# Kernel tuning notes

Measured on AMD Instinct MI355X. Metric: run time of the kernel, lower is better.

## Reference

```python
import jax, jax.numpy as jnp
import numpy as np

# Fixed architecture constants (match init_kwargs)
B, CIN, H, W = 2, 3, 224, 224
COUT = 64
KH = KW = 7
SH = SW = 2
PAD = 3
GROUPS = 1
MIX = 4
CG = COUT // GROUPS          # channels per group
REL = CG // 2                # rel_size
PH, PW = H + 2 * PAD, W + 2 * PAD          # padded spatial dims (230, 230)
FH = (PH - KH) // SH + 1                    # output height (112)
FW = (PW - KW) // SW + 1                    # output width  (112)


def setup_inputs() -> dict:
    key = jax.random.key(0)
    ks = jax.random.split(key, 10)
    n = jax.random.normal
    return {
        "x": n(ks[0], (B, CIN, H, W), jnp.float32),
        "weight_query": n(ks[1], (GROUPS, CIN // GROUPS, CG), jnp.float32) * 0.2,
        "weight_key": n(ks[2], (GROUPS, CIN // GROUPS, CG), jnp.float32) * 0.2,
        "weight_value": n(ks[3], (MIX, GROUPS, CIN // GROUPS, CG), jnp.float32) * 0.2,
        "relative_x": n(ks[4], (REL, 1, KW), jnp.float32) * 0.1,
        "relative_y": n(ks[5], (CG - REL, KH, 1), jnp.float32) * 0.1,
        "emb_x": n(ks[6], (CG, 1, PW), jnp.float32) * 0.1,
        "emb_y": n(ks[7], (CG, PH, 1), jnp.float32) * 0.1,
        "emb_m": n(ks[8], (MIX, CG, 1, 1), jnp.float32) * 0.1,
        "bias": n(ks[9], (COUT,), jnp.float32) * 0.05,
    }


def _unfold(t):
    """torch.nn.functional.unfold: (b,c,PH,PW) -> (b,c,KH*KW,FH*FW) with (c,kh,kw) layout."""
    b, c = t.shape[0], t.shape[1]
    ri = jnp.arange(FH) * SH
    rj = jnp.arange(FW) * SW
    p = t[:, :, ri[:, None] + jnp.arange(KH)[None, :], :]          # (b,c,FH,KH,PW)
    p = p[:, :, :, :, rj[:, None] + jnp.arange(KW)[None, :]]       # (b,c,FH,KH,FW,KW)
    return p.transpose(0, 1, 3, 5, 2, 4).reshape(b, c, KH * KW, FH * FW)


def _forward(x, wq, wk, wv, rx, ry, ex, ey, em, bias):
    b = x.shape[0]
    # relative position bias: (COUT, KH*KW, 1)
    rel = jnp.concatenate([jnp.tile(rx, (1, KH, 1)), jnp.tile(ry, (1, 1, KW))], axis=0)
    rel = jnp.tile(rel, (GROUPS, 1, 1)).reshape(COUT, KH * KW, 1)

    xp = jnp.pad(x, ((0, 0), (0, 0), (PAD, PAD), (PAD, PAD)))       # (b,CIN,PH,PW)
    x_ij = xp.transpose(0, 2, 3, 1).reshape(b, PH * PW, GROUPS, CIN // GROUPS)

    # per-pixel grouped projections -> (b, COUT, PH, PW)
    vq = jnp.einsum('bngi,gio->bgon', x_ij, wq).reshape(b, COUT, PH, PW)
    vk = jnp.einsum('bngi,gio->bgon', x_ij, wk).reshape(b, COUT, PH, PW)

    # mixture weights over value transforms: softmax over mix axis, per pixel
    p_ab = ex + ey                                                   # (CG,PH,PW)
    p_abm = jax.nn.softmax(jnp.sum(p_ab[None] * em, axis=1), axis=0) # (MIX,PH,PW)

    vvm = jnp.einsum('bngi,mgio->mbgon', x_ij, wv).reshape(MIX, b, COUT, PH, PW)
    vv = jnp.sum(vvm * p_abm[:, None, None], axis=0)                 # (b,COUT,PH,PW)

    win_k = _unfold(vk)                                              # (b,COUT,KH*KW,L)
    win_v = _unfold(vv)                                              # (b,COUT,KH*KW,L)
    # center query of each window (equivalent to unfold then slice center)
    ci = (KH - 1) // 2 + jnp.arange(FH) * SH
    cj = (KW - 1) // 2 + jnp.arange(FW) * SW
    win_q = vq[:, :, ci[:, None], cj[None, :]].reshape(b, COUT, 1, FH * FW)

    scores = jnp.sum(win_q * (win_k + rel[None]), axis=1)            # (b,KH*KW,L)
    # NOTE: the torch code applies softmax over dim=2 which, after the sum over
    # channels, is the SPATIAL dim (L), not the window dim. Faithful to source.
    attn = jax.nn.softmax(scores, axis=2)                            # (b,KH*KW,L)
    v = jnp.sum(attn[:, None] * win_v, axis=2) + bias[None, :, None] # (b,COUT,L)
    return v.reshape(b, COUT, FH, FW)


def reference(x, weight_query, weight_key, weight_value, relative_x, relative_y, emb_x, emb_y, emb_m, bias):
    return _forward(x, weight_query, weight_key, weight_value, relative_x, relative_y, emb_x, emb_y, emb_m, bias)
```

## Files before the change

### kernel.cpp

```cpp
#include <hip/hip_runtime.h>
#include <math.h>

namespace {
constexpr int Bc = 2, Hc = 224, Wc = 224, HWc = Hc * Wc;
constexpr int COUTc = 64, PADc = 3;
constexpr int MIXc = 4, RELc = 32;
constexpr int PHc = 230, PWc = 230;
constexpr int FHc = 112, FWc = 112, NN = FHc * FWc;
constexpr int NK = 49;
constexpr int CH = 32;
constexpr int NCH = NN / CH;
constexpr int WS_EEX = 0;
constexpr int WS_EEY = WS_EEX + MIXc * PWc;
constexpr int WS_PART = WS_EEY + MIXc * PHc;
constexpr int WS_E = WS_PART + Bc * NK * NCH;
}

__device__ __forceinline__ void collapse(const float* __restrict__ wq,
                                         const float* __restrict__ wk,
                                         const float* __restrict__ rx,
                                         const float* __restrict__ ry,
                                         float* sCol) {
  const int t = threadIdx.x;
  if (t < 51) {
    float s = 0.f;
    if (t < 9) {
      const int cj = t / 3, ci = t % 3;
#pragma unroll 8
      for (int o = 0; o < COUTc; ++o) s += wq[cj * COUTc + o] * wk[ci * COUTc + o];
    } else if (t < 30) {
      const int v = t - 9, cj = v / 7, kw = v % 7;
#pragma unroll 8
      for (int o = 0; o < RELc; ++o) s += wq[cj * COUTc + o] * rx[o * 7 + kw];
    } else {
      const int v = t - 30, cj = v / 7, kh = v % 7;
#pragma unroll 8
      for (int o = 0; o < RELc; ++o) s += wq[cj * COUTc + RELc + o] * ry[o * 7 + kh];
    }
    sCol[t] = s;
  }
}

__global__ __launch_bounds__(256) void sam_scores(
    const float* __restrict__ x, const float* __restrict__ wq,
    const float* __restrict__ wk, const float* __restrict__ rx,
    const float* __restrict__ ry, const float* __restrict__ ex,
    const float* __restrict__ ey, const float* __restrict__ em,
    float* __restrict__ ws) {
  __shared__ float sCol[51];
  const int t = threadIdx.x;
  const int c = blockIdx.x, b = blockIdx.y;
  collapse(wq, wk, rx, ry, sCol);

  const int bf = b * NCH + c;
  if (bf < 8) {
    const int idx = bf * 256 + t;
    constexpr int half = MIXc * PWc;
    if (idx < 2 * half) {
      const int which = idx >= half;
      const int r = which ? idx - half : idx;
      const int m = r / PWc, j = r % PWc;
      float s = 0.f;
#pragma unroll 8
      for (int cc = 0; cc < COUTc; ++cc)
        s += (which ? ey[cc * PHc + j] : ex[cc * PWc + j]) * em[m * COUTc + cc];
      ws[idx] = __expf(s);
    }
  }
  __syncthreads();

  const int g = t >> 5, px = t & 31;
  const int n = c * CH + px;
  const int fh = n / FWc, fw = n - fh * FWc;
  const int i0 = 2 * fh, j0 = 2 * fw;
  const float* xb = x + (size_t)b * 3 * HWc;
  const int co = i0 * Wc + j0;
  const float xc0 = xb[co], xc1 = xb[HWc + co], xc2 = xb[2 * HWc + co];
  const float q0 = xc0 * sCol[0] + xc1 * sCol[3] + xc2 * sCol[6];
  const float q1 = xc0 * sCol[1] + xc1 * sCol[4] + xc2 * sCol[7];
  const float q2 = xc0 * sCol[2] + xc1 * sCol[5] + xc2 * sCol[8];

  float* E = ws + WS_E;
  float* part = ws + WS_PART;
#pragma unroll
  for (int it = 0; it < 7; ++it) {
    const int kk = g + 8 * it;
    if (kk < NK) {
      const int kh = kk / 7, kw = kk - 7 * kh;
      float s = xc0 * (sCol[9 + kw] + sCol[30 + kh]) +
                xc1 * (sCol[16 + kw] + sCol[37 + kh]) +
                xc2 * (sCol[23 + kw] + sCol[44 + kh]);
      const int ir = i0 + kh - PADc, jc = j0 + kw - PADc;
      if ((unsigned)ir < (unsigned)Hc && (unsigned)jc < (unsigned)Wc) {
        const int off = ir * Wc + jc;
        s += q0 * xb[off] + q1 * xb[HWc + off] + q2 * xb[2 * HWc + off];
      }
      const float e = __expf(s);
      E[(size_t)(b * NK + kk) * NN + n] = e;
      float r = e;
      r += __shfl_xor(r, 1, 64);
      r += __shfl_xor(r, 2, 64);
      r += __shfl_xor(r, 4, 64);
      r += __shfl_xor(r, 8, 64);
      r += __shfl_xor(r, 16, 64);
      if (px == 0) part[(b * NK + kk) * NCH + c] = r;
    }
  }
}

__global__ __launch_bounds__(256) void sam_out(
    const float* __restrict__ x, const float* __restrict__ wv,
    const float* __restrict__ bias, const float* __restrict__ ws,
    float* __restrict__ out) {
  __shared__ float sEEX[MIXc * PWc];
  __shared__ float sEEY[MIXc * PHc];
  __shared__ float sdninv[NK];
  __shared__ float swv[12 * 64];
  __shared__ float sbias[64];
  __shared__ float sT[8][32][13];

  const int t = threadIdx.x;
  const int c = blockIdx.x, b = blockIdx.y;
  for (int i = t; i < MIXc * PWc; i += 256) sEEX[i] = ws[WS_EEX + i];
  for (int i = t; i < MIXc * PHc; i += 256) sEEY[i] = ws[WS_EEY + i];
  if (t < 64) sbias[t] = bias[t];
  for (int i = t; i < 12 * 64; i += 256) swv[i] = wv[i];
  if (t < 4 * NK) {
    const int k = t >> 2, p = t & 3;
    const float* base = ws + WS_PART + (b * NK + k) * NCH;
    float s = 0.f;
    for (int cc = p; cc < NCH; cc += 4) s += base[cc];
    s += __shfl_xor(s, 1, 64);
    s += __shfl_xor(s, 2, 64);
    if (p == 0) sdninv[k] = 1.f / s;
  }
  __syncthreads();

  const int g = t >> 5, px = t & 31;
  const int n = c * CH + px;
  const int fh = n / FWc, fw = n - fh * FWc;
  const int i0 = 2 * fh, j0 = 2 * fw;
  const float* xb = x + (size_t)b * 3 * HWc;
  const float* E = ws + WS_E;

  float T[12] = {0.f};
#pragma unroll
  for (int it = 0; it < 7; ++it) {
    const int kk = g + 8 * it;
    if (kk < NK) {
      const int kh = kk / 7, kw = kk - 7 * kh;
      const int ir = i0 + kh - PADc, jc = j0 + kw - PADc;
      if ((unsigned)ir < (unsigned)Hc && (unsigned)jc < (unsigned)Wc) {
        const float e = E[(size_t)(b * NK + kk) * NN + n] * sdninv[kk];
        const int ii = i0 + kh, jj = j0 + kw;
        const float p0 = sEEX[jj] * sEEY[ii];
        const float p1 = sEEX[PWc + jj] * sEEY[PHc + ii];
        const float p2 = sEEX[2 * PWc + jj] * sEEY[2 * PHc + ii];
        const float p3 = sEEX[3 * PWc + jj] * sEEY[3 * PHc + ii];
        const float wgt = e * __builtin_amdgcn_rcpf(p0 + p1 + p2 + p3);
        const int off = ir * Wc + jc;
        const float x0 = xb[off], x1 = xb[HWc + off], x2 = xb[2 * HWc + off];
        const float a0 = wgt * p0, a1 = wgt * p1, a2 = wgt * p2, a3 = wgt * p3;
        T[0] += a0 * x0; T[1]  += a0 * x1; T[2]  += a0 * x2;
        T[3] += a1 * x0; T[4]  += a1 * x1; T[5]  += a1 * x2;
        T[6] += a2 * x0; T[7]  += a2 * x1; T[8]  += a2 * x2;
        T[9] += a3 * x0; T[10] += a3 * x1; T[11] += a3 * x2;
      }
    }
  }
#pragma unroll
  for (int j = 0; j < 12; ++j) sT[g][px][j] = T[j];
  __syncthreads();

  float Tm[12];
#pragma unroll
  for (int j = 0; j < 12; ++j) {
    float s = 0.f;
#pragma unroll
    for (int ww = 0; ww < 8; ++ww) s += sT[ww][px][j];
    Tm[j] = s;
  }
  float* ob = out + (size_t)b * COUTc * NN + n;
#pragma unroll
  for (int oo = 0; oo < 8; ++oo) {
    const int o = g * 8 + oo;
    float acc = sbias[o];
#pragma unroll
    for (int mc = 0; mc < 12; ++mc) acc += swv[mc * 64 + o] * Tm[mc];
    ob[(size_t)o * NN] = acc;
  }
}

extern "C" void kernel_launch(void* const* d_in, const int* in_sizes, int n_in,
                              void* d_out, int out_size, void* d_ws, size_t ws_size,
                              hipStream_t stream) {
  const float* x    = (const float*)d_in[0];
  const float* wq   = (const float*)d_in[1];
  const float* wk   = (const float*)d_in[2];
  const float* wv   = (const float*)d_in[3];
  const float* rx   = (const float*)d_in[4];
  const float* ry   = (const float*)d_in[5];
  const float* ex   = (const float*)d_in[6];
  const float* ey   = (const float*)d_in[7];
  const float* em   = (const float*)d_in[8];
  const float* bias = (const float*)d_in[9];
  float* out = (float*)d_out;
  float* ws  = (float*)d_ws;

  sam_scores<<<dim3(NCH, Bc), 256, 0, stream>>>(x, wq, wk, rx, ry, ex, ey, em, ws);
  sam_out<<<dim3(NCH, Bc), 256, 0, stream>>>(x, wv, bias, ws, out);
}
```

Before: 113.2 us.

## Recompute attention exponentials in output kernel instead of storing them

The stats kernel now only computes per-chunk partial sums of the exponentiated scores, with a new grid over (chunk, kernel-offset group, batch) and 64-pixel chunks. It no longer writes the full (B,49,N) exponential tensor to workspace. The output kernel recomputes the collapsed weights and each exponential from x, reusing the x loads it already needs. This removes a large global write and read round-trip at the cost of extra exp and arithmetic work, and of repeating the weight collapse in every block.

```diff
diff --git a/kernel.cpp b/kernel.cpp
--- a/kernel.cpp
+++ b/kernel.cpp
@@ -8,12 +8,10 @@
 constexpr int PHc = 230, PWc = 230;
 constexpr int FHc = 112, FWc = 112, NN = FHc * FWc;
 constexpr int NK = 49;
-constexpr int CH = 32;
-constexpr int NCH = NN / CH;
+constexpr int NCHUNK = 196;
 constexpr int WS_EEX = 0;
 constexpr int WS_EEY = WS_EEX + MIXc * PWc;
 constexpr int WS_PART = WS_EEY + MIXc * PHc;
-constexpr int WS_E = WS_PART + Bc * NK * NCH;
 }
 
 __device__ __forceinline__ void collapse(const float* __restrict__ wq,
@@ -41,7 +39,7 @@
   }
 }
 
-__global__ __launch_bounds__(256) void sam_scores(
+__global__ __launch_bounds__(256) void sam_stats(
     const float* __restrict__ x, const float* __restrict__ wq,
     const float* __restrict__ wk, const float* __restrict__ rx,
     const float* __restrict__ ry, const float* __restrict__ ex,
@@ -49,12 +47,10 @@
     float* __restrict__ ws) {
   __shared__ float sCol[51];
   const int t = threadIdx.x;
-  const int c = blockIdx.x, b = blockIdx.y;
   collapse(wq, wk, rx, ry, sCol);
 
-  const int bf = b * NCH + c;
-  if (bf < 8) {
-    const int idx = bf * 256 + t;
+  if (blockIdx.y == 0 && blockIdx.z == 0 && blockIdx.x < 8) {
+    const int idx = blockIdx.x * 256 + t;
     constexpr int half = MIXc * PWc;
     if (idx < 2 * half) {
       const int which = idx >= half;
@@ -69,8 +65,69 @@
   }
   __syncthreads();
 
+  const int w = t >> 6, lane = t & 63;
+  const int k = blockIdx.y * 4 + w;
+  if (k >= NK) return;
+  const int b = blockIdx.z;
+  const int kh = k / 7, kw = k - 7 * kh;
+  const int n = blockIdx.x * 64 + lane;
+  const int fh = n / FWc, fw = n - fh * FWc;
+  const int i0 = 2 * fh, j0 = 2 * fw;
+  const float* xb = x + (size_t)b * 3 * HWc;
+  const int co = i0 * Wc + j0;
+  const float xc0 = xb[co], xc1 = xb[HWc + co], xc2 = xb[2 * HWc + co];
+
+  float s = xc0 * (sCol[9 + kw] + sCol[30 + kh]) +
+            xc1 * (sCol[16 + kw] + sCol[37 + kh]) +
+            xc2 * (sCol[23 + kw] + sCol[44 + kh]);
+  const int ir = i0 + kh - PADc, jc = j0 + kw - PADc;
+  if ((unsigned)ir < (unsigned)Hc && (unsigned)jc < (unsigned)Wc) {
+    const float q0 = xc0 * sCol[0] + xc1 * sCol[3] + xc2 * sCol[6];
+    const float q1 = xc0 * sCol[1] + xc1 * sCol[4] + xc2 * sCol[7];
+    const float q2 = xc0 * sCol[2] + xc1 * sCol[5] + xc2 * sCol[8];
+    const int off = ir * Wc + jc;
+    s += q0 * xb[off] + q1 * xb[HWc + off] + q2 * xb[2 * HWc + off];
+  }
+  float e = __expf(s);
+#pragma unroll
+  for (int m2 = 32; m2; m2 >>= 1) e += __shfl_xor(e, m2, 64);
+  if (lane == 0) ws[WS_PART + (b * NK + k) * NCHUNK + blockIdx.x] = e;
+}
+
+__global__ __launch_bounds__(256) void sam_out(
+    const float* __restrict__ x, const float* __restrict__ wq,
+    const float* __restrict__ wk, const float* __restrict__ rx,
+    const float* __restrict__ ry, const float* __restrict__ wv,
+    const float* __restrict__ bias, const float* __restrict__ ws,
+    float* __restrict__ out) {
+  __shared__ float sCol[51];
+  __shared__ float sEEX[MIXc * PWc];
+  __shared__ float sEEY[MIXc * PHc];
+  __shared__ float sdninv[NK];
+  __shared__ float swv[12 * 64];
+  __shared__ float sbias[64];
+  __shared__ float sT[8][32][13];
+
+  const int t = threadIdx.x;
+  const int c = blockIdx.x, b = blockIdx.y;
+  collapse(wq, wk, rx, ry, sCol);
+  for (int i = t; i < MIXc * PWc; i += 256) sEEX[i] = ws[WS_EEX + i];
+  for (int i = t; i < MIXc * PHc; i += 256) sEEY[i] = ws[WS_EEY + i];
+  if (t < 64) sbias[t] = bias[t];
+  for (int i = t; i < 12 * 64; i += 256) swv[i] = wv[i];
+  if (t < 4 * NK) {
+    const int k = t >> 2, p = t & 3;
+    const float* base = ws + WS_PART + (b * NK + k) * NCHUNK;
+    float s = 0.f;
+    for (int cc = p; cc < NCHUNK; cc += 4) s += base[cc];
+    s += __shfl_xor(s, 1, 64);
+    s += __shfl_xor(s, 2, 64);
+    if (p == 0) sdninv[k] = 1.f / s;
+  }
+  __syncthreads();
+
   const int g = t >> 5, px = t & 31;
-  const int n = c * CH + px;
+  const int n = c * 32 + px;
   const int fh = n / FWc, fw = n - fh * FWc;
   const int i0 = 2 * fh, j0 = 2 * fw;
   const float* xb = x + (size_t)b * 3 * HWc;
@@ -80,69 +137,6 @@
   const float q1 = xc0 * sCol[1] + xc1 * sCol[4] + xc2 * sCol[7];
   const float q2 = xc0 * sCol[2] + xc1 * sCol[5] + xc2 * sCol[8];
 
-  float* E = ws + WS_E;
-  float* part = ws + WS_PART;
-#pragma unroll
-  for (int it = 0; it < 7; ++it) {
-    const int kk = g + 8 * it;
-    if (kk < NK) {
-      const int kh = kk / 7, kw = kk - 7 * kh;
-      float s = xc0 * (sCol[9 + kw] + sCol[30 + kh]) +
-                xc1 * (sCol[16 + kw] + sCol[37 + kh]) +
-                xc2 * (sCol[23 + kw] + sCol[44 + kh]);
-      const int ir = i0 + kh - PADc, jc = j0 + kw - PADc;
-      if ((unsigned)ir < (unsigned)Hc && (unsigned)jc < (unsigned)Wc) {
-        const int off = ir * Wc + jc;
-        s += q0 * xb[off] + q1 * xb[HWc + off] + q2 * xb[2 * HWc + off];
-      }
-      const float e = __expf(s);
-      E[(size_t)(b * NK + kk) * NN + n] = e;
-      float r = e;
-      r += __shfl_xor(r, 1, 64);
-      r += __shfl_xor(r, 2, 64);
-      r += __shfl_xor(r, 4, 64);
-      r += __shfl_xor(r, 8, 64);
-      r += __shfl_xor(r, 16, 64);
-      if (px == 0) part[(b * NK + kk) * NCH + c] = r;
-    }
-  }
-}
-
-__global__ __launch_bounds__(256) void sam_out(
-    const float* __restrict__ x, const float* __restrict__ wv,
-    const float* __restrict__ bias, const float* __restrict__ ws,
-    float* __restrict__ out) {
-  __shared__ float sEEX[MIXc * PWc];
-  __shared__ float sEEY[MIXc * PHc];
-  __shared__ float sdninv[NK];
-  __shared__ float swv[12 * 64];
-  __shared__ float sbias[64];
-  __shared__ float sT[8][32][13];
-
-  const int t = threadIdx.x;
-  const int c = blockIdx.x, b = blockIdx.y;
-  for (int i = t; i < MIXc * PWc; i += 256) sEEX[i] = ws[WS_EEX + i];
-  for (int i = t; i < MIXc * PHc; i += 256) sEEY[i] = ws[WS_EEY + i];
-  if (t < 64) sbias[t] = bias[t];
-  for (int i = t; i < 12 * 64; i += 256) swv[i] = wv[i];
-  if (t < 4 * NK) {
-    const int k = t >> 2, p = t & 3;
-    const float* base = ws + WS_PART + (b * NK + k) * NCH;
-    float s = 0.f;
-    for (int cc = p; cc < NCH; cc += 4) s += base[cc];
-    s += __shfl_xor(s, 1, 64);
-    s += __shfl_xor(s, 2, 64);
-    if (p == 0) sdninv[k] = 1.f / s;
-  }
-  __syncthreads();
-
-  const int g = t >> 5, px = t & 31;
-  const int n = c * CH + px;
-  const int fh = n / FWc, fw = n - fh * FWc;
-  const int i0 = 2 * fh, j0 = 2 * fw;
-  const float* xb = x + (size_t)b * 3 * HWc;
-  const float* E = ws + WS_E;
-
   float T[12] = {0.f};
 #pragma unroll
   for (int it = 0; it < 7; ++it) {
@@ -151,15 +145,19 @@
       const int kh = kk / 7, kw = kk - 7 * kh;
       const int ir = i0 + kh - PADc, jc = j0 + kw - PADc;
       if ((unsigned)ir < (unsigned)Hc && (unsigned)jc < (unsigned)Wc) {
-        const float e = E[(size_t)(b * NK + kk) * NN + n] * sdninv[kk];
+        float s = xc0 * (sCol[9 + kw] + sCol[30 + kh]) +
+                  xc1 * (sCol[16 + kw] + sCol[37 + kh]) +
+                  xc2 * (sCol[23 + kw] + sCol[44 + kh]);
+        const int off = ir * Wc + jc;
+        const float x0 = xb[off], x1 = xb[HWc + off], x2 = xb[2 * HWc + off];
+        s += q0 * x0 + q1 * x1 + q2 * x2;
+        const float e = __expf(s) * sdninv[kk];
         const int ii = i0 + kh, jj = j0 + kw;
         const float p0 = sEEX[jj] * sEEY[ii];
         const float p1 = sEEX[PWc + jj] * sEEY[PHc + ii];
         const float p2 = sEEX[2 * PWc + jj] * sEEY[2 * PHc + ii];
         const float p3 = sEEX[3 * PWc + jj] * sEEY[3 * PHc + ii];
         const float wgt = e * __builtin_amdgcn_rcpf(p0 + p1 + p2 + p3);
-        const int off = ir * Wc + jc;
-        const float x0 = xb[off], x1 = xb[HWc + off], x2 = xb[2 * HWc + off];
         const float a0 = wgt * p0, a1 = wgt * p1, a2 = wgt * p2, a3 = wgt * p3;
         T[0] += a0 * x0; T[1]  += a0 * x1; T[2]  += a0 * x2;
         T[3] += a1 * x0; T[4]  += a1 * x1; T[5]  += a1 * x2;
@@ -207,6 +205,8 @@
   float* out = (float*)d_out;
   float* ws  = (float*)d_ws;
 
-  sam_scores<<<dim3(NCH, Bc), 256, 0, stream>>>(x, wq, wk, rx, ry, ex, ey, em, ws);
-  sam_out<<<dim3(NCH, Bc), 256, 0, stream>>>(x, wv, bias, ws, out);
-}
+  sam_stats<<<dim3(NCHUNK, 13, Bc), 256, 0, stream>>>(x, wq, wk, rx, ry, ex, ey,
+                                                      em, ws);
+  sam_out<<<dim3(NN / 32, Bc), 256, 0, stream>>>(x, wq, wk, rx, ry, wv, bias,
+                                                 ws, out);
+}
```

Measured after the change: 119.3 us. 5.4% more time.
